# Kernel tuning notes

Hardware: AMD Instinct MI355X
Metric: run time of the kernel (lower is better)

The kernel has to match this reference:

```python
import jax, jax.numpy as jnp
import numpy as np

IN_SIZE = 1024
OUT_SIZE = 3 * IN_SIZE  # must equal 3*in_size for trigger_a * attn broadcast
B, S = 32, 512


def setup_inputs() -> dict:
    key = jax.random.key(0)
    ks = jax.random.split(key, 8)
    h_state = jax.random.normal(ks[0], (B, S, 2 * IN_SIZE), dtype=jnp.float32)
    x = jax.random.normal(ks[1], (B, S, IN_SIZE), dtype=jnp.float32)
    trigger = jax.random.randint(ks[2], (B,), 0, S)
    mask = jax.random.randint(ks[3], (B, S), 0, 2).astype(jnp.int32)
    # learned params (nn.Linear: y = x @ W.T + b; store pre-transposed as (in, out))
    Wa = jax.random.normal(ks[4], (3 * IN_SIZE, OUT_SIZE), dtype=jnp.float32) / np.sqrt(3 * IN_SIZE)
    ba = jnp.zeros((OUT_SIZE,), dtype=jnp.float32)
    Ws = jax.random.normal(ks[5], (2 * IN_SIZE, OUT_SIZE), dtype=jnp.float32) / np.sqrt(2 * IN_SIZE)
    bs = jnp.zeros((OUT_SIZE,), dtype=jnp.float32)
    return {"h_state": h_state, "x": x, "trigger": trigger, "mask": mask,
            "Wa": Wa, "ba": ba, "Ws": Ws, "bs": bs}


def reference(h_state, x, trigger, mask, Wa, ba, Ws, bs):
    # a: (B, S, 3*in_size)
    a = jnp.concatenate([h_state, x], axis=-1)
    b = a.shape[0]
    # one_hot + masked_select in the original == gather of the trigger row per batch
    trigger_a = a[jnp.arange(b), trigger]  # (B, 3*in_size)
    s = h_state.sum(axis=1)  # (B, 2*in_size)
    # et: (B, S, out_size)
    et = jnp.tanh(a @ Wa + ba + (s @ Ws + bs)[:, None, :])
    # masked_fill where mask == 0 (mask broadcast over feature dim)
    et = jnp.where(mask[:, :, None] == 0, jnp.float32(-1e9), et)
    # softmax over the FEATURE dim (dim=-1), as in the original; dropout in eval mode is identity
    attn = jax.nn.softmax(et, axis=-1)
    # trigger-weighted reduction over the sequence dim
    out = (trigger_a[:, None, :] * attn).sum(axis=1)  # (B, out_size)
    return out
```

## Files before the change

### kernel.cpp

```cpp
#include <hip/hip_runtime.h>
#include <hip/hip_bf16.h>
#include <hip/hip_fp16.h>


namespace {
constexpr int SIN  = 1024;
constexpr int KH   = 2048;
constexpr int NF   = 3072;
constexpr int NBAT = 32;
constexpr int NS   = 512;
constexpr int NM   = NBAT * NS;
constexpr int NDB  = NF / 64;
constexpr int KC   = 8;
constexpr int NKT  = NF / 64;
constexpr int NCH  = 8;
}

typedef unsigned short u16;
typedef __bf16 bf16x8 __attribute__((ext_vector_type(8)));
typedef float  f32x4  __attribute__((ext_vector_type(4)));

#define ASYNC_CP16(gptr, lptr)                                                              \
  __builtin_amdgcn_global_load_lds((__attribute__((address_space(1))) void*)(gptr),         \
                                   (__attribute__((address_space(3))) void*)(lptr), 16, 0, 0)

__device__ __forceinline__ u16 f2b(float f) {
  union { float f; unsigned u; } v; v.f = f;
  unsigned u = v.u;
  u += 0x7FFFu + ((u >> 16) & 1u);
  return (u16)(u >> 16);
}

__global__ __launch_bounds__(64) void k_cnt(const int* __restrict__ mask,
                                            int* __restrict__ bcnt) {
  int b = blockIdx.x, t = threadIdx.x;
  int c = 0;
#pragma unroll
  for (int i = 0; i < NS / 64; ++i) c += mask[b * NS + i * 64 + t];
#pragma unroll
  for (int off = 32; off >= 1; off >>= 1) c += __shfl_down(c, off, 64);
  if (t == 0) bcnt[b] = c;
}

__global__ __launch_bounds__(64) void k_scan(const int* __restrict__ bcnt,
                                             int* __restrict__ boff,
                                             int* __restrict__ meta) {
  if (threadIdx.x == 0) {
    int run = 0;
    for (int b = 0; b < NBAT; ++b) { boff[b] = run; run += bcnt[b]; }
    meta[0] = run;
    meta[1] = (run + 255) & ~255;
  }
}

__global__ __launch_bounds__(512) void k_gather(const int* __restrict__ mask,
                                                const int* __restrict__ boff,
                                                const int* __restrict__ meta,
                                                int* __restrict__ rowmap) {
  __shared__ int ps[NS];
  int b = blockIdx.x, t = threadIdx.x;
  int m = mask[b * NS + t];
  ps[t] = m;
  __syncthreads();
#pragma unroll
  for (int off = 1; off < NS; off <<= 1) {
    int v = (t >= off) ? ps[t - off] : 0;
    __syncthreads();
    ps[t] += v;
    __syncthreads();
  }
  if (m) rowmap[boff[b] + ps[t] - m] = b * NS + t;
  if (b == 0) {
    int Mc = meta[0], McPad = meta[1];
    if (Mc + t < McPad) rowmap[Mc + t] = 0;
  }
}

__global__ __launch_bounds__(256) void k_sum_h(const float* __restrict__ h,
                                               float* __restrict__ s) {
  int b = blockIdx.x;
  int d = blockIdx.y * 256 + threadIdx.x;
  const float* p = h + (size_t)b * NS * KH + d;
  float acc = 0.f;
#pragma unroll 8
  for (int t = 0; t < NS; ++t) acc += p[(size_t)t * KH];
  s[b * KH + d] = acc;
}

__global__ __launch_bounds__(256) void k_base1(const float* __restrict__ s,
                                               const float* __restrict__ Ws,
                                               float* __restrict__ basep) {
  __shared__ float sT[NBAT][KH / KC];
  int f  = blockIdx.x * 256 + threadIdx.x;
  int k0 = blockIdx.y * (KH / KC);
  for (int it = 0; it < NBAT; ++it) {
    int idx = it * 256 + threadIdx.x;
    int b = idx >> 8, kk = idx & 255;
    sT[b][kk] = s[b * KH + k0 + kk];
  }
  __syncthreads();
  float acc[NBAT] = {};
  for (int k = 0; k < KH / KC; ++k) {
    float w = Ws[(size_t)(k0 + k) * NF + f];
#pragma unroll
    for (int b = 0; b < NBAT; ++b) acc[b] += sT[b][k] * w;
  }
#pragma unroll
  for (int b = 0; b < NBAT; ++b)
    basep[((size_t)blockIdx.y * NBAT + b) * NF + f] = acc[b];
}

__global__ __launch_bounds__(256) void k_base2(const float* __restrict__ basep,
                                               const float* __restrict__ ba,
                                               const float* __restrict__ bs,
                                               float* __restrict__ base) {
  int b = blockIdx.x;
  int f = blockIdx.y * 256 + threadIdx.x;
  float acc = 0.f;
#pragma unroll
  for (int kc = 0; kc < KC; ++kc) acc += basep[((size_t)kc * NBAT + b) * NF + f];
  base[b * NF + f] = acc + ba[f] + bs[f];
}

__global__ __launch_bounds__(256) void k_cvt_a(const float* __restrict__ h,
                                               const float* __restrict__ x,
                                               const int* __restrict__ rowmap,
                                               const int* __restrict__ meta,
                                               u16* __restrict__ A) {
  int tid = blockIdx.x * 256 + threadIdx.x;
  int i = tid / (NF / 4);
  if (i >= meta[1]) return;
  int k = (tid - i * (NF / 4)) * 4;
  ushort4 o;
  if (i >= meta[0]) {
    o.x = o.y = o.z = o.w = 0;
  } else {
    int ro = rowmap[i];
    int b = ro >> 9, t = ro & 511;
    const float* src = (k < KH) ? h + ((size_t)b * NS + t) * KH + k
                                : x + ((size_t)b * NS + t) * SIN + (k - KH);
    float4 v = *(const float4*)src;
    o.x = f2b(v.x); o.y = f2b(v.y); o.z = f2b(v.z); o.w = f2b(v.w);
  }
  *(ushort4*)(A + (size_t)i * NF + k) = o;
}

__global__ __launch_bounds__(256) void k_wat(const float* __restrict__ Wa,
                                             u16* __restrict__ WaT) {
  __shared__ float tile[64][65];
  int k0 = blockIdx.x * 64, f0 = blockIdx.y * 64;
  int tid = threadIdx.x;
  int col4 = (tid & 15) * 4, row = tid >> 4;
#pragma unroll
  for (int rr = 0; rr < 64; rr += 16) {
    float4 v = *(const float4*)(Wa + (size_t)(k0 + row + rr) * NF + f0 + col4);
    tile[row + rr][col4 + 0] = v.x; tile[row + rr][col4 + 1] = v.y;
    tile[row + rr][col4 + 2] = v.z; tile[row + rr][col4 + 3] = v.w;
  }
  __syncthreads();
#pragma unroll
  for (int rr = 0; rr < 64; rr += 16) {
    int f = f0 + row + rr;
    ushort4 o;
    o.x = f2b(tile[col4 + 0][row + rr]); o.y = f2b(tile[col4 + 1][row + rr]);
    o.z = f2b(tile[col4 + 2][row + rr]); o.w = f2b(tile[col4 + 3][row + rr]);
    *(ushort4*)(WaT + (size_t)f * NF + k0 + col4) = o;
  }
}

#define LDSOFF(row, gg) ((row) * 32 + ((((gg) ^ (((row) >> 1) & 3))) << 3))

#define LDB4(BUF, KS)                                                        \
  _Pragma("unroll") for (int nf = 0; nf < 4; ++nf) {                         \
    int rb = wc * 64 + nf * 16 + lr;                                         \
    bfr[nf] = *(const bf16x8*)&lds[BUF][1][KS][LDSOFF(rb, g)];               \
  }

#define LDA4(BUF, KS, MH)                                                    \
  _Pragma("unroll") for (int mf = 0; mf < 4; ++mf) {                         \
    int ra = wr * 128 + ((MH) * 4 + mf) * 16 + lr;                           \
    afr[mf] = *(const bf16x8*)&lds[BUF][0][KS][LDSOFF(ra, g)];               \
  }

#define MFMA16(MH)                                                           \
  _Pragma("unroll") for (int mf = 0; mf < 4; ++mf)                           \
  _Pragma("unroll") for (int nf = 0; nf < 4; ++nf)                           \
    acc[(MH) * 4 + mf][nf] = __builtin_amdgcn_mfma_f32_16x16x32_bf16(        \
        afr[mf], bfr[nf], acc[(MH) * 4 + mf][nf], 0, 0, 0);

#define STAGE(SMAT, SBUF, SKS, SKT)                                          \
  if ((SKT) < NKT) {                                                         \
    _Pragma("unroll") for (int q = 0; q < 2; ++q) {                          \
      const u16* src = ((SMAT) ? pB[q] : pA[q]) + (SKT) * 64 + (SKS) * 32;   \
      ASYNC_CP16(src, &lds[SBUF][SMAT][SKS][q * 4096 + wid * 512]);          \
    }                                                                        \
  }

#define PH(BUF, KS, MH, SMAT, SBUF, SKS, SKT)                                \
  {                                                                          \
    if ((MH) == 0) { LDB4(BUF, KS) }                                         \
    LDA4(BUF, KS, MH)                                                        \
    STAGE(SMAT, SBUF, SKS, SKT)                                              \
    __builtin_amdgcn_s_setprio(1);                                           \
    MFMA16(MH)                                                               \
    __builtin_amdgcn_s_setprio(0);                                           \
    asm volatile("s_waitcnt vmcnt(6)" ::: "memory");                         \
    __builtin_amdgcn_s_barrier();                                            \
  }

__global__ __launch_bounds__(512, 2) void k_gemm(const u16* __restrict__ A,
                                                 const u16* __restrict__ Wt,
                                                 const float* __restrict__ base,
                                                 const int* __restrict__ rowmap,
                                                 const int* __restrict__ meta,
                                                 __half* __restrict__ P,
                                                 float* __restrict__ Dpart) {
  __shared__ __align__(16) u16 lds[2][2][2][8192];
  const int MT   = meta[1] >> 8;
  const int nact = MT * 12;
  const int flat = blockIdx.x;
  if (flat >= nact) return;
  const int qx = nact >> 3, rx = nact & 7;
  const int xcd = flat & 7, idx = flat >> 3;
  const int swz = (xcd < rx) ? xcd * (qx + 1) + idx
                             : rx * (qx + 1) + (xcd - rx) * qx + idx;
  const int mt = swz / 12, nt = swz - mt * 12;
  const int r0 = mt << 8, c0 = nt << 8;

  const int tid = threadIdx.x;
  const int wid = tid >> 6, lane = tid & 63;
  const int wr = wid >> 2, wc = wid & 3;
  const int g = lane >> 4, lr = lane & 15;

  const u16* pA[2]; const u16* pB[2];
#pragma unroll
  for (int q = 0; q < 2; ++q) {
    int c = q * 512 + tid;
    int row = c >> 2;
    int kc8 = (((c & 3) ^ ((row >> 1) & 3)) << 3);
    pA[q] = A  + (size_t)(r0 + row) * NF + kc8;
    pB[q] = Wt + (size_t)(c0 + row) * NF + kc8;
  }

  f32x4 acc[8][4] = {};
  bf16x8 afr[4], bfr[4];

  STAGE(0, 0, 0, 0) STAGE(1, 0, 0, 0)
  STAGE(0, 0, 1, 0) STAGE(1, 0, 1, 0)
  STAGE(0, 1, 0, 1) STAGE(1, 1, 0, 1)
  asm volatile("s_waitcnt vmcnt(8)" ::: "memory");
  __builtin_amdgcn_s_barrier();

#pragma unroll 1
  for (int i = 0; i < NKT / 2; ++i) {
    const int kt1 = 2 * i + 1, kt2 = 2 * i + 2, kt3 = 2 * i + 3;
    PH(0, 0, 0, 0, 1, 1, kt1)
    PH(0, 0, 1, 1, 1, 1, kt1)
    PH(0, 1, 0, 0, 0, 0, kt2)
    PH(0, 1, 1, 1, 0, 0, kt2)
    PH(1, 0, 0, 0, 0, 1, kt2)
    PH(1, 0, 1, 1, 0, 1, kt2)
    PH(1, 1, 0, 0, 1, 0, kt3)
    PH(1, 1, 1, 1, 1, 0, kt3)
  }

  const int cbase = c0 + wc * 64;
#pragma unroll
  for (int mf = 0; mf < 8; ++mf) {
#pragma unroll
    for (int j = 0; j < 4; ++j) {
      int i = r0 + wr * 128 + mf * 16 + g * 4 + j;
      int b = rowmap[i] >> 9;
      float rs = 0.f;
#pragma unroll
      for (int nf = 0; nf < 4; ++nf) {
        int ccn = cbase + nf * 16 + lr;
        float z  = acc[mf][nf][j] + base[b * NF + ccn];
        z        = fminf(fmaxf(z, -15.f), 15.f);
        float e2 = __expf(2.f * z);
        float th = (e2 - 1.f) / (e2 + 1.f);
        float p  = __expf(th);
        P[(size_t)i * NF + ccn] = __float2half(p);
        rs += p;
      }
#pragma unroll
      for (int off = 1; off < 16; off <<= 1) rs += __shfl_xor(rs, off, 64);
      if (lr == 0) Dpart[(size_t)i * NDB + (cbase >> 6)] = rs;
    }
  }
}

__global__ __launch_bounds__(256) void k_invd(const float* __restrict__ Dpart,
                                              const int* __restrict__ meta,
                                              float* __restrict__ invD) {
  int i = blockIdx.x * 256 + threadIdx.x;
  if (i >= meta[1]) return;
  float d = 0.f;
#pragma unroll
  for (int q = 0; q < NDB; ++q) d += Dpart[(size_t)i * NDB + q];
  invD[i] = 1.0f / d;
}

__global__ __launch_bounds__(256) void k_final1(const __half* __restrict__ P,
                                                const float* __restrict__ invD,
                                                const int* __restrict__ boff,
                                                const int* __restrict__ bcnt,
                                                float* __restrict__ pb) {
  int c = blockIdx.x;
  int b = c >> 3, j = c & 7;
  int f = blockIdx.y * 256 + threadIdx.x;
  int cnt = bcnt[b];
  int lo = j * 64, hi = min(cnt, lo + 64);
  int off = boff[b];
  float acc = 0.f;
  for (int t = lo; t < hi; ++t)
    acc += __half2float(P[(size_t)(off + t) * NF + f]) * invD[off + t];
  pb[(size_t)c * NF + f] = acc;
}

__global__ __launch_bounds__(256) void k_final2(const float* __restrict__ pb,
                                                const int* __restrict__ bcnt,
                                                const float* __restrict__ h,
                                                const float* __restrict__ x,
                                                const int* __restrict__ trig,
                                                float* __restrict__ out) {
  int b = blockIdx.x;
  int f = blockIdx.y * 256 + threadIdx.x;
  float acc = 0.f;
#pragma unroll
  for (int j = 0; j < NCH; ++j) acc += pb[(size_t)(b * NCH + j) * NF + f];
  acc += (float)(NS - bcnt[b]) * (1.0f / (float)NF);
  int tr = trig[b];
  float ta = (f < KH) ? h[((size_t)b * NS + tr) * KH + f]
                      : x[((size_t)b * NS + tr) * SIN + f - KH];
  out[b * NF + f] = acc * ta;
}

extern "C" void kernel_launch(void* const* d_in, const int* in_sizes, int n_in,
                              void* d_out, int out_size, void* d_ws, size_t ws_size,
                              hipStream_t stream) {
  const float* h_state = (const float*)d_in[0];
  const float* x       = (const float*)d_in[1];
  const int*   trigger = (const int*)d_in[2];
  const int*   mask    = (const int*)d_in[3];
  const float* Wa      = (const float*)d_in[4];
  const float* ba      = (const float*)d_in[5];
  const float* Ws      = (const float*)d_in[6];
  const float* bs      = (const float*)d_in[7];
  float*       out     = (float*)d_out;

  char* w = (char*)d_ws;
  u16*    Abf   = (u16*)w;                 w += (size_t)NM * NF * 2;
  u16*    WaT   = (u16*)w;                 w += (size_t)NF * NF * 2;
  __half* P     = (__half*)w;              w += (size_t)NM * NF * 2;
  float*  s     = (float*)w;               w += (size_t)NBAT * KH * 4;
  float*  base  = (float*)w;               w += (size_t)NBAT * NF * 4;
  float*  Dpart = (float*)w;               w += (size_t)NM * NDB * 4;
  float*  basep = (float*)Dpart;
  float*  pb    = (float*)Dpart;
  float*  invD  = (float*)w;               w += (size_t)NM * 4;
  int*    rowmap= (int*)w;                 w += (size_t)NM * 4;
  int*    bcnt  = (int*)w;                 w += 128;
  int*    boff  = (int*)w;                 w += 128;
  int*    meta  = (int*)w;                 w += 128;

  (void)in_sizes; (void)n_in; (void)out_size; (void)ws_size;

  k_cnt   <<<dim3(NBAT), 64, 0, stream>>>(mask, bcnt);
  k_scan  <<<dim3(1), 64, 0, stream>>>(bcnt, boff, meta);
  k_gather<<<dim3(NBAT), 512, 0, stream>>>(mask, boff, meta, rowmap);
  k_sum_h <<<dim3(NBAT, KH / 256), 256, 0, stream>>>(h_state, s);
  k_cvt_a <<<dim3(NM * (NF / 4) / 256), 256, 0, stream>>>(h_state, x, rowmap, meta, Abf);
  k_wat   <<<dim3(NF / 64, NF / 64), 256, 0, stream>>>(Wa, WaT);
  k_base1 <<<dim3(NF / 256, KC), 256, 0, stream>>>(s, Ws, basep);
  k_base2 <<<dim3(NBAT, NF / 256), 256, 0, stream>>>(basep, ba, bs, base);
  k_gemm  <<<dim3((NF / 256) * (NM / 256)), 512, 0, stream>>>(Abf, WaT, base, rowmap, meta, P, Dpart);
  k_invd  <<<dim3(NM / 256), 256, 0, stream>>>(Dpart, meta, invD);
  k_final1<<<dim3(NBAT * NCH, NF / 256), 256, 0, stream>>>(P, invD, boff, bcnt, pb);
  k_final2<<<dim3(NBAT, NF / 256), 256, 0, stream>>>(pb, bcnt, h_state, x, trigger, out);
}
```

Baseline: 417.0 us.

## Merge count/scan kernels, grid-stride cvt_a, vectorize final1 with half2 loads

Fuses the mask count and the prefix scan into one single-block kernel, which saves one launch. Converts the activation cast kernel to a fixed 2048-block grid-stride loop sized by the compacted row count, so blocks for rows dropped by compaction are no longer launched. Vectorizes the final reduction to handle two features per thread with half2 loads and caches the inverse denominators in shared memory, halving that grid. These are small tail-kernel optimizations around the dominant GEMM.

```diff
diff --git a/kernel.cpp b/kernel.cpp
--- a/kernel.cpp
+++ b/kernel.cpp
@@ -31,23 +31,24 @@
   return (u16)(u >> 16);
 }
 
-__global__ __launch_bounds__(64) void k_cnt(const int* __restrict__ mask,
-                                            int* __restrict__ bcnt) {
-  int b = blockIdx.x, t = threadIdx.x;
+__global__ __launch_bounds__(256) void k_prep(const int* __restrict__ mask,
+                                              int* __restrict__ bcnt,
+                                              int* __restrict__ boff,
+                                              int* __restrict__ meta) {
+  int tid = threadIdx.x;
+  int b = tid >> 3, seg = tid & 7;
   int c = 0;
 #pragma unroll
-  for (int i = 0; i < NS / 64; ++i) c += mask[b * NS + i * 64 + t];
-#pragma unroll
-  for (int off = 32; off >= 1; off >>= 1) c += __shfl_down(c, off, 64);
-  if (t == 0) bcnt[b] = c;
-}
-
-__global__ __launch_bounds__(64) void k_scan(const int* __restrict__ bcnt,
-                                             int* __restrict__ boff,
-                                             int* __restrict__ meta) {
-  if (threadIdx.x == 0) {
+  for (int i = 0; i < 64; ++i) c += mask[b * NS + seg * 64 + i];
+  c += __shfl_xor(c, 1, 64);
+  c += __shfl_xor(c, 2, 64);
+  c += __shfl_xor(c, 4, 64);
+  __shared__ int sc[NBAT];
+  if (seg == 0) { sc[b] = c; bcnt[b] = c; }
+  __syncthreads();
+  if (tid == 0) {
     int run = 0;
-    for (int b = 0; b < NBAT; ++b) { boff[b] = run; run += bcnt[b]; }
+    for (int bb = 0; bb < NBAT; ++bb) { boff[bb] = run; run += sc[bb]; }
     meta[0] = run;
     meta[1] = (run + 255) & ~255;
   }
@@ -127,22 +128,24 @@
                                                const int* __restrict__ rowmap,
                                                const int* __restrict__ meta,
                                                u16* __restrict__ A) {
-  int tid = blockIdx.x * 256 + threadIdx.x;
-  int i = tid / (NF / 4);
-  if (i >= meta[1]) return;
-  int k = (tid - i * (NF / 4)) * 4;
-  ushort4 o;
-  if (i >= meta[0]) {
-    o.x = o.y = o.z = o.w = 0;
-  } else {
-    int ro = rowmap[i];
-    int b = ro >> 9, t = ro & 511;
-    const float* src = (k < KH) ? h + ((size_t)b * NS + t) * KH + k
-                                : x + ((size_t)b * NS + t) * SIN + (k - KH);
-    float4 v = *(const float4*)src;
-    o.x = f2b(v.x); o.y = f2b(v.y); o.z = f2b(v.z); o.w = f2b(v.w);
-  }
-  *(ushort4*)(A + (size_t)i * NF + k) = o;
+  const int total = meta[1] * (NF / 4);
+  for (int idx = blockIdx.x * 256 + threadIdx.x; idx < total;
+       idx += gridDim.x * 256) {
+    int i = idx / (NF / 4);
+    int k = (idx - i * (NF / 4)) * 4;
+    ushort4 o;
+    if (i >= meta[0]) {
+      o.x = o.y = o.z = o.w = 0;
+    } else {
+      int ro = rowmap[i];
+      int b = ro >> 9, t = ro & 511;
+      const float* src = (k < KH) ? h + ((size_t)b * NS + t) * KH + k
+                                  : x + ((size_t)b * NS + t) * SIN + (k - KH);
+      float4 v = *(const float4*)src;
+      o.x = f2b(v.x); o.y = f2b(v.y); o.z = f2b(v.z); o.w = f2b(v.w);
+    }
+    *(ushort4*)(A + (size_t)i * NF + k) = o;
+  }
 }
 
 __global__ __launch_bounds__(256) void k_wat(const float* __restrict__ Wa,
@@ -308,14 +311,23 @@
                                                 float* __restrict__ pb) {
   int c = blockIdx.x;
   int b = c >> 3, j = c & 7;
-  int f = blockIdx.y * 256 + threadIdx.x;
+  int f = blockIdx.y * 512 + threadIdx.x * 2;
   int cnt = bcnt[b];
   int lo = j * 64, hi = min(cnt, lo + 64);
   int off = boff[b];
-  float acc = 0.f;
-  for (int t = lo; t < hi; ++t)
-    acc += __half2float(P[(size_t)(off + t) * NF + f]) * invD[off + t];
-  pb[(size_t)c * NF + f] = acc;
+  __shared__ float ivs[64];
+  if (threadIdx.x < 64 && lo + (int)threadIdx.x < hi)
+    ivs[threadIdx.x] = invD[off + lo + threadIdx.x];
+  __syncthreads();
+  float ax = 0.f, ay = 0.f;
+  for (int t = lo; t < hi; ++t) {
+    __half2 hv = *(const __half2*)(P + (size_t)(off + t) * NF + f);
+    float2 fv = __half22float2(hv);
+    float iv = ivs[t - lo];
+    ax += fv.x * iv; ay += fv.y * iv;
+  }
+  float2 o; o.x = ax; o.y = ay;
+  *(float2*)(pb + (size_t)c * NF + f) = o;
 }
 
 __global__ __launch_bounds__(256) void k_final2(const float* __restrict__ pb,
@@ -366,16 +378,15 @@
 
   (void)in_sizes; (void)n_in; (void)out_size; (void)ws_size;
 
-  k_cnt   <<<dim3(NBAT), 64, 0, stream>>>(mask, bcnt);
-  k_scan  <<<dim3(1), 64, 0, stream>>>(bcnt, boff, meta);
+  k_prep  <<<dim3(1), 256, 0, stream>>>(mask, bcnt, boff, meta);
   k_gather<<<dim3(NBAT), 512, 0, stream>>>(mask, boff, meta, rowmap);
   k_sum_h <<<dim3(NBAT, KH / 256), 256, 0, stream>>>(h_state, s);
-  k_cvt_a <<<dim3(NM * (NF / 4) / 256), 256, 0, stream>>>(h_state, x, rowmap, meta, Abf);
+  k_cvt_a <<<dim3(2048), 256, 0, stream>>>(h_state, x, rowmap, meta, Abf);
   k_wat   <<<dim3(NF / 64, NF / 64), 256, 0, stream>>>(Wa, WaT);
   k_base1 <<<dim3(NF / 256, KC), 256, 0, stream>>>(s, Ws, basep);
   k_base2 <<<dim3(NBAT, NF / 256), 256, 0, stream>>>(basep, ba, bs, base);
   k_gemm  <<<dim3((NF / 256) * (NM / 256)), 512, 0, stream>>>(Abf, WaT, base, rowmap, meta, P, Dpart);
   k_invd  <<<dim3(NM / 256), 256, 0, stream>>>(Dpart, meta, invD);
-  k_final1<<<dim3(NBAT * NCH, NF / 256), 256, 0, stream>>>(P, invD, boff, bcnt, pb);
+  k_final1<<<dim3(NBAT * NCH, NF / 512), 256, 0, stream>>>(P, invD, boff, bcnt, pb);
   k_final2<<<dim3(NBAT, NF / 256), 256, 0, stream>>>(pb, bcnt, h_state, x, trigger, out);
 }
```

New measurement: 399.0 us. 1.05x faster.
